# Kernel tuning notes

Hardware: AMD Instinct MI355X
Metric: run time of the kernel (lower is better)

Reference implementation:

```python
import jax, jax.numpy as jnp
import numpy as np

N_NODES = 50000
N_EDGES = 800000
D = 64


def setup_inputs() -> dict:
    key = jax.random.key(0)
    k1, k2, k3 = jax.random.split(key, 3)
    x = jax.random.normal(k1, (N_NODES, D), dtype=jnp.float32)
    edge_index = jax.random.randint(k2, (2, N_EDGES), 0, N_NODES, dtype=jnp.int64)
    # GCNConv linear weight (PyG stores lin.weight [out, in]; we use [in, out])
    W = jax.random.normal(k3, (D, D), dtype=jnp.float32) * (1.0 / np.sqrt(D))
    b = jnp.zeros((D,), dtype=jnp.float32)
    return {"x": x, "edge_index": edge_index, "W": W, "b": b}


def reference(x, edge_index, W, b):
    # ResidualGCNLayer forward (eval mode: dropout = identity).
    # in_channels == out_channels -> skip_connection is Identity.
    N = x.shape[0]
    E = edge_index.shape[1]
    dtype = x.dtype

    # GCNConv with add_self_loops=True, improved=False (fill value 1.0)
    loop = jnp.arange(N, dtype=edge_index.dtype)
    row = jnp.concatenate([edge_index[0], loop])  # source nodes
    col = jnp.concatenate([edge_index[1], loop])  # destination nodes
    ew = jnp.ones((E + N,), dtype=dtype)          # edge weights (self-loop fill=1)

    # symmetric normalization: D^{-1/2} A_hat D^{-1/2}
    deg = jax.ops.segment_sum(ew, col, num_segments=N)
    dinv = jnp.where(deg > 0, jax.lax.rsqrt(deg), jnp.zeros_like(deg))
    norm = dinv[row] * ew * dinv[col]             # [E+N]

    h = x @ W                                     # [N, D] transform before propagate
    msg = norm[:, None] * h[row]                  # [E+N, D] gathered + scaled messages
    agg = jax.ops.segment_sum(msg, col, num_segments=N)  # scatter-add aggregate

    identity = x                                  # Identity skip (in == out)
    out = jax.nn.relu(agg + b) + identity         # ReLU + (eval) dropout + residual
    return out
```

## Files before the change

### kernel.cpp

```cpp
#include <hip/hip_runtime.h>
#include <hip/hip_bf16.h>

#define D 64
#define CAP 64
#define NXCD 8
#define EPT 4

typedef int v4i __attribute__((ext_vector_type(4)));

__device__ __forceinline__ float bf16lo(unsigned u) {
    u <<= 16; return __builtin_bit_cast(float, u);
}
__device__ __forceinline__ float bf16hi(unsigned u) {
    u &= 0xffff0000u; return __builtin_bit_cast(float, u);
}
__device__ __forceinline__ unsigned bf16_rne(float f) {
    unsigned u = __builtin_bit_cast(unsigned, f);
    u += 0x7fffu + ((u >> 16) & 1u);
    return u >> 16;
}
__device__ __forceinline__ unsigned pack_bf16(float a, float b) {
    return bf16_rne(a) | (bf16_rne(b) << 16);
}

__global__ void zero_cnt_kernel(int* __restrict__ cnt, int N) {
    int i = blockIdx.x * blockDim.x + threadIdx.x;
    if (i < N) cnt[i] = 0;
}

__global__ __launch_bounds__(256) void fill_csr_sliced_kernel(
        const int* __restrict__ row, const int* __restrict__ col,
        int* __restrict__ cnt, int* __restrict__ csr, int E, int N) {
    const int slice = blockIdx.x & (NXCD - 1);
    const int chunk = blockIdx.x >> 3;
    const int per = (N + NXCD - 1) / NXCD;
    const int lo = slice * per;
    const int hi = min(N, lo + per);

    const int e0 = (chunk * 256 + (int)threadIdx.x) * EPT;
    if (e0 + EPT <= E) {
        v4i c4 = __builtin_nontemporal_load((const v4i*)(col + e0));
        #pragma unroll
        for (int i = 0; i < EPT; ++i) {
            int c = c4[i];
            if (c >= lo && c < hi) {
                int r = __builtin_nontemporal_load(row + e0 + i);
                int pos = atomicAdd(&cnt[c], 1);
                if (pos < CAP) csr[c * CAP + pos] = r;
            }
        }
    } else {
        for (int i = 0; i < EPT; ++i) {
            int e = e0 + i;
            if (e < E) {
                int c = col[e];
                if (c >= lo && c < hi) {
                    int pos = atomicAdd(&cnt[c], 1);
                    if (pos < CAP) csr[c * CAP + pos] = row[e];
                }
            }
        }
    }
}

__global__ __launch_bounds__(256) void transform_kernel(
        const float* __restrict__ x, const float* __restrict__ W,
        const int* __restrict__ cnt, unsigned* __restrict__ h2b, int N) {
    __shared__ float Ws[D * D];
    __shared__ float xs[32][68];

    for (int i = threadIdx.x; i < D * D; i += 256) Ws[i] = W[i];

    const int l16 = threadIdx.x & 15;
    const int m   = threadIdx.x >> 4;
    const int base = blockIdx.x * 64;
    const float4* x4 = (const float4*)x;

    for (int pass = 0; pass < 2; ++pass) {
        int nb = base + pass * 32;
        __syncthreads();
        for (int i = threadIdx.x; i < 512; i += 256) {
            int r = i >> 4, seg = i & 15;
            int n = nb + r;
            float4 v = make_float4(0.f, 0.f, 0.f, 0.f);
            if (n < N) v = x4[n * 16 + seg];
            *(float4*)&xs[r][seg * 4] = v;
        }
        __syncthreads();

        float4 acc0 = make_float4(0.f, 0.f, 0.f, 0.f);
        float4 acc1 = make_float4(0.f, 0.f, 0.f, 0.f);
        #pragma unroll 4
        for (int k4 = 0; k4 < 16; ++k4) {
            float4 xv0 = *(const float4*)&xs[m][k4 * 4];
            float4 xv1 = *(const float4*)&xs[m + 16][k4 * 4];
            #pragma unroll
            for (int kk = 0; kk < 4; ++kk) {
                float4 w4 = *(const float4*)&Ws[(k4 * 4 + kk) * D + l16 * 4];
                float a0 = kk == 0 ? xv0.x : kk == 1 ? xv0.y : kk == 2 ? xv0.z : xv0.w;
                float a1 = kk == 0 ? xv1.x : kk == 1 ? xv1.y : kk == 2 ? xv1.z : xv1.w;
                acc0.x = fmaf(a0, w4.x, acc0.x); acc0.y = fmaf(a0, w4.y, acc0.y);
                acc0.z = fmaf(a0, w4.z, acc0.z); acc0.w = fmaf(a0, w4.w, acc0.w);
                acc1.x = fmaf(a1, w4.x, acc1.x); acc1.y = fmaf(a1, w4.y, acc1.y);
                acc1.z = fmaf(a1, w4.z, acc1.z); acc1.w = fmaf(a1, w4.w, acc1.w);
            }
        }

        int n0 = nb + m, n1 = nb + m + 16;
        if (n0 < N) {
            float dn = rsqrtf((float)(cnt[n0] + 1));
            uint2 p; p.x = pack_bf16(acc0.x * dn, acc0.y * dn);
            p.y = pack_bf16(acc0.z * dn, acc0.w * dn);
            ((uint2*)h2b)[n0 * 16 + l16] = p;
        }
        if (n1 < N) {
            float dn = rsqrtf((float)(cnt[n1] + 1));
            uint2 p; p.x = pack_bf16(acc1.x * dn, acc1.y * dn);
            p.y = pack_bf16(acc1.z * dn, acc1.w * dn);
            ((uint2*)h2b)[n1 * 16 + l16] = p;
        }
    }
}

__global__ __launch_bounds__(256) void agg_kernel(
        const float* __restrict__ x, const float* __restrict__ b,
        const unsigned* __restrict__ h2b, const int* __restrict__ cnt,
        const int* __restrict__ csr, float* __restrict__ out, int N) {
    const int l16 = threadIdx.x & 15;
    const int gid = threadIdx.x >> 4;
    const int gw  = gid & 3;
    const int c = blockIdx.x * 16 + gid;
    if (c >= N) return;

    const uint2* hb = (const uint2*)h2b;

    const float4 bv = ((const float4*)b)[l16];
    const float4 xv = ((const float4*)x)[c * 16 + l16];

    uint2 v = hb[c * 16 + l16];
    float4 acc;
    acc.x = bf16lo(v.x); acc.y = bf16hi(v.x);
    acc.z = bf16lo(v.y); acc.w = bf16hi(v.y);

    int n = cnt[c]; n = n < CAP ? n : CAP;
    const int* cb = csr + c * CAP;

    for (int j0 = 0; j0 < n; j0 += 16) {
        int idx = (j0 + l16 < n) ? cb[j0 + l16] : 0;
        int m = n - j0; m = m < 16 ? m : 16;
        #pragma unroll 4
        for (int jj = 0; jj < m; ++jj) {
            int r = __shfl(idx, gw * 16 + jj);
            uint2 w = hb[r * 16 + l16];
            acc.x += bf16lo(w.x); acc.y += bf16hi(w.x);
            acc.z += bf16lo(w.y); acc.w += bf16hi(w.y);
        }
    }

    float dc = rsqrtf((float)(cnt[c] + 1));
    float4 o;
    o.x = fmaf(dc, acc.x, bv.x); o.x = o.x > 0.0f ? o.x : 0.0f; o.x += xv.x;
    o.y = fmaf(dc, acc.y, bv.y); o.y = o.y > 0.0f ? o.y : 0.0f; o.y += xv.y;
    o.z = fmaf(dc, acc.z, bv.z); o.z = o.z > 0.0f ? o.z : 0.0f; o.z += xv.z;
    o.w = fmaf(dc, acc.w, bv.w); o.w = o.w > 0.0f ? o.w : 0.0f; o.w += xv.w;
    ((float4*)out)[c * 16 + l16] = o;
}

extern "C" void kernel_launch(void* const* d_in, const int* in_sizes, int n_in,
                              void* d_out, int out_size, void* d_ws, size_t ws_size,
                              hipStream_t stream) {
    const float* x   = (const float*)d_in[0];
    const int*   ei  = (const int*)d_in[1];
    const float* W   = (const float*)d_in[2];
    const float* b   = (const float*)d_in[3];
    float*       out = (float*)d_out;

    const int N = in_sizes[0] / D;
    const int E = in_sizes[1] / 2;
    const int* row = ei;
    const int* col = ei + E;

    int*      cnt = (int*)d_ws;
    unsigned* h2b = (unsigned*)(cnt + N);
    int*      csr = (int*)(h2b + (size_t)N * D / 2);

    zero_cnt_kernel<<<(N + 255) / 256, 256, 0, stream>>>(cnt, N);

    const int fill_chunks = (E + 256 * EPT - 1) / (256 * EPT);
    fill_csr_sliced_kernel<<<fill_chunks * NXCD, 256, 0, stream>>>(row, col, cnt, csr, E, N);

    transform_kernel<<<(N + 63) / 64, 256, 0, stream>>>(x, W, cnt, h2b, N);
    agg_kernel<<<(N + 15) / 16, 256, 0, stream>>>(x, b, h2b, cnt, csr, out, N);
}
```

Baseline: 156.5 us.

## Fuse four graph-conv kernels into one persistent kernel with grid barriers

Replaces the zero, CSR-fill, transform and aggregate launches with a single persistent kernel of 1024 blocks that loops over the work of each phase and separates phases with a software grid barrier built on an atomic counter. The aim is to remove per-launch overhead and the gaps between the four dispatches. The barrier relies on all 1024 blocks being co-resident, which a normal launch does not guarantee, so it could deadlock. Grid-wide barriers and fewer blocks in the fill and aggregate phases may also cost more than the launch gaps they remove.

Result: slower. 563.7 us (+260.3%).

```diff
diff --git a/kernel.cpp b/kernel.cpp
--- a/kernel.cpp
+++ b/kernel.cpp
@@ -5,6 +5,8 @@
 #define CAP 64
 #define NXCD 8
 #define EPT 4
+#define GRID 1024
+#define TPB 256
 
 typedef int v4i __attribute__((ext_vector_type(4)));
 
@@ -23,147 +25,168 @@
     return bf16_rne(a) | (bf16_rne(b) << 16);
 }
 
-__global__ void zero_cnt_kernel(int* __restrict__ cnt, int N) {
-    int i = blockIdx.x * blockDim.x + threadIdx.x;
-    if (i < N) cnt[i] = 0;
-}
-
-__global__ __launch_bounds__(256) void fill_csr_sliced_kernel(
-        const int* __restrict__ row, const int* __restrict__ col,
-        int* __restrict__ cnt, int* __restrict__ csr, int E, int N) {
-    const int slice = blockIdx.x & (NXCD - 1);
-    const int chunk = blockIdx.x >> 3;
-    const int per = (N + NXCD - 1) / NXCD;
-    const int lo = slice * per;
-    const int hi = min(N, lo + per);
-
-    const int e0 = (chunk * 256 + (int)threadIdx.x) * EPT;
-    if (e0 + EPT <= E) {
-        v4i c4 = __builtin_nontemporal_load((const v4i*)(col + e0));
-        #pragma unroll
-        for (int i = 0; i < EPT; ++i) {
-            int c = c4[i];
-            if (c >= lo && c < hi) {
-                int r = __builtin_nontemporal_load(row + e0 + i);
-                int pos = atomicAdd(&cnt[c], 1);
-                if (pos < CAP) csr[c * CAP + pos] = r;
+__device__ __forceinline__ void grid_sync(unsigned* bar, unsigned target) {
+    __syncthreads();
+    if (threadIdx.x == 0) {
+        __threadfence();
+        atomicAdd(bar, 1u);
+        while (__hip_atomic_load(bar, __ATOMIC_ACQUIRE,
+                                 __HIP_MEMORY_SCOPE_AGENT) < target)
+            __builtin_amdgcn_s_sleep(8);
+        __threadfence();
+    }
+    __syncthreads();
+}
+
+__global__ __launch_bounds__(TPB, 4) void fused_kernel(
+        const float* __restrict__ x, const int* __restrict__ row,
+        const int* __restrict__ col, const float* __restrict__ W,
+        const float* __restrict__ b, int* __restrict__ cnt,
+        unsigned* __restrict__ h2b, int* __restrict__ csr,
+        unsigned* __restrict__ bar, float* __restrict__ out,
+        int N, int E) {
+    __shared__ float Ws[D * D];
+    __shared__ float xs[32][68];
+
+    const int tid = threadIdx.x;
+
+    for (int i = blockIdx.x * TPB + tid; i < N; i += GRID * TPB) cnt[i] = 0;
+    grid_sync(bar, GRID * 1u);
+
+    {
+        const int per = (N + NXCD - 1) / NXCD;
+        const int nch = (E + TPB * EPT - 1) / (TPB * EPT);
+        for (int vw = blockIdx.x; vw < nch * NXCD; vw += GRID) {
+            const int slice = vw & (NXCD - 1);
+            const int chunk = vw >> 3;
+            const int lo = slice * per;
+            const int hi = min(N, lo + per);
+            const int e0 = (chunk * TPB + tid) * EPT;
+            if (e0 + EPT <= E) {
+                v4i c4 = __builtin_nontemporal_load((const v4i*)(col + e0));
+                #pragma unroll
+                for (int i = 0; i < EPT; ++i) {
+                    int c = c4[i];
+                    if (c >= lo && c < hi) {
+                        int r = __builtin_nontemporal_load(row + e0 + i);
+                        int pos = atomicAdd(&cnt[c], 1);
+                        if (pos < CAP) csr[c * CAP + pos] = r;
+                    }
+                }
+            } else {
+                for (int i = 0; i < EPT; ++i) {
+                    int e = e0 + i;
+                    if (e < E) {
+                        int c = col[e];
+                        if (c >= lo && c < hi) {
+                            int pos = atomicAdd(&cnt[c], 1);
+                            if (pos < CAP) csr[c * CAP + pos] = row[e];
+                        }
+                    }
+                }
             }
         }
-    } else {
-        for (int i = 0; i < EPT; ++i) {
-            int e = e0 + i;
-            if (e < E) {
-                int c = col[e];
-                if (c >= lo && c < hi) {
-                    int pos = atomicAdd(&cnt[c], 1);
-                    if (pos < CAP) csr[c * CAP + pos] = row[e];
+    }
+    grid_sync(bar, GRID * 2u);
+
+    for (int i = tid; i < D * D; i += TPB) Ws[i] = W[i];
+    {
+        const int l16 = tid & 15;
+        const int m   = tid >> 4;
+        const float4* x4 = (const float4*)x;
+        const int ntiles = (N + 63) / 64;
+        for (int tile = blockIdx.x; tile < ntiles; tile += GRID) {
+            const int base = tile * 64;
+            for (int pass = 0; pass < 2; ++pass) {
+                int nb = base + pass * 32;
+                __syncthreads();
+                for (int i = tid; i < 512; i += TPB) {
+                    int r = i >> 4, seg = i & 15;
+                    int n = nb + r;
+                    float4 v = make_float4(0.f, 0.f, 0.f, 0.f);
+                    if (n < N) v = x4[n * 16 + seg];
+                    *(float4*)&xs[r][seg * 4] = v;
+                }
+                __syncthreads();
+
+                float4 acc0 = make_float4(0.f, 0.f, 0.f, 0.f);
+                float4 acc1 = make_float4(0.f, 0.f, 0.f, 0.f);
+                #pragma unroll 4
+                for (int k4 = 0; k4 < 16; ++k4) {
+                    float4 xv0 = *(const float4*)&xs[m][k4 * 4];
+                    float4 xv1 = *(const float4*)&xs[m + 16][k4 * 4];
+                    #pragma unroll
+                    for (int kk = 0; kk < 4; ++kk) {
+                        float4 w4 = *(const float4*)&Ws[(k4 * 4 + kk) * D + l16 * 4];
+                        float a0 = kk == 0 ? xv0.x : kk == 1 ? xv0.y : kk == 2 ? xv0.z : xv0.w;
+                        float a1 = kk == 0 ? xv1.x : kk == 1 ? xv1.y : kk == 2 ? xv1.z : xv1.w;
+                        acc0.x = fmaf(a0, w4.x, acc0.x); acc0.y = fmaf(a0, w4.y, acc0.y);
+                        acc0.z = fmaf(a0, w4.z, acc0.z); acc0.w = fmaf(a0, w4.w, acc0.w);
+                        acc1.x = fmaf(a1, w4.x, acc1.x); acc1.y = fmaf(a1, w4.y, acc1.y);
+                        acc1.w = fmaf(a1, w4.w, acc1.w); acc1.z = fmaf(a1, w4.z, acc1.z);
+                    }
+                }
+
+                int n0 = nb + m, n1 = nb + m + 16;
+                if (n0 < N) {
+                    float dn = rsqrtf((float)(cnt[n0] + 1));
+                    uint2 p; p.x = pack_bf16(acc0.x * dn, acc0.y * dn);
+                    p.y = pack_bf16(acc0.z * dn, acc0.w * dn);
+                    ((uint2*)h2b)[n0 * 16 + l16] = p;
+                }
+                if (n1 < N) {
+                    float dn = rsqrtf((float)(cnt[n1] + 1));
+                    uint2 p; p.x = pack_bf16(acc1.x * dn, acc1.y * dn);
+                    p.y = pack_bf16(acc1.z * dn, acc1.w * dn);
+                    ((uint2*)h2b)[n1 * 16 + l16] = p;
                 }
             }
         }
     }
-}
-
-__global__ __launch_bounds__(256) void transform_kernel(
-        const float* __restrict__ x, const float* __restrict__ W,
-        const int* __restrict__ cnt, unsigned* __restrict__ h2b, int N) {
-    __shared__ float Ws[D * D];
-    __shared__ float xs[32][68];
-
-    for (int i = threadIdx.x; i < D * D; i += 256) Ws[i] = W[i];
-
-    const int l16 = threadIdx.x & 15;
-    const int m   = threadIdx.x >> 4;
-    const int base = blockIdx.x * 64;
-    const float4* x4 = (const float4*)x;
-
-    for (int pass = 0; pass < 2; ++pass) {
-        int nb = base + pass * 32;
-        __syncthreads();
-        for (int i = threadIdx.x; i < 512; i += 256) {
-            int r = i >> 4, seg = i & 15;
-            int n = nb + r;
-            float4 v = make_float4(0.f, 0.f, 0.f, 0.f);
-            if (n < N) v = x4[n * 16 + seg];
-            *(float4*)&xs[r][seg * 4] = v;
-        }
-        __syncthreads();
-
-        float4 acc0 = make_float4(0.f, 0.f, 0.f, 0.f);
-        float4 acc1 = make_float4(0.f, 0.f, 0.f, 0.f);
-        #pragma unroll 4
-        for (int k4 = 0; k4 < 16; ++k4) {
-            float4 xv0 = *(const float4*)&xs[m][k4 * 4];
-            float4 xv1 = *(const float4*)&xs[m + 16][k4 * 4];
-            #pragma unroll
-            for (int kk = 0; kk < 4; ++kk) {
-                float4 w4 = *(const float4*)&Ws[(k4 * 4 + kk) * D + l16 * 4];
-                float a0 = kk == 0 ? xv0.x : kk == 1 ? xv0.y : kk == 2 ? xv0.z : xv0.w;
-                float a1 = kk == 0 ? xv1.x : kk == 1 ? xv1.y : kk == 2 ? xv1.z : xv1.w;
-                acc0.x = fmaf(a0, w4.x, acc0.x); acc0.y = fmaf(a0, w4.y, acc0.y);
-                acc0.z = fmaf(a0, w4.z, acc0.z); acc0.w = fmaf(a0, w4.w, acc0.w);
-                acc1.x = fmaf(a1, w4.x, acc1.x); acc1.y = fmaf(a1, w4.y, acc1.y);
-                acc1.z = fmaf(a1, w4.z, acc1.z); acc1.w = fmaf(a1, w4.w, acc1.w);
+    grid_sync(bar, GRID * 3u);
+
+    {
+        const int l16 = tid & 15;
+        const int gid = tid >> 4;
+        const int gw  = gid & 3;
+        const uint2* hb = (const uint2*)h2b;
+        const int ntiles = (N + 15) / 16;
+        for (int tile = blockIdx.x; tile < ntiles; tile += GRID) {
+            const int c = tile * 16 + gid;
+            if (c < N) {
+                const float4 bv = ((const float4*)b)[l16];
+                const float4 xv = ((const float4*)x)[c * 16 + l16];
+
+                uint2 v = hb[c * 16 + l16];
+                float4 acc;
+                acc.x = bf16lo(v.x); acc.y = bf16hi(v.x);
+                acc.z = bf16lo(v.y); acc.w = bf16hi(v.y);
+
+                int n = cnt[c]; n = n < CAP ? n : CAP;
+                const int* cb = csr + c * CAP;
+
+                for (int j0 = 0; j0 < n; j0 += 16) {
+                    int idx = (j0 + l16 < n) ? cb[j0 + l16] : 0;
+                    int m = n - j0; m = m < 16 ? m : 16;
+                    #pragma unroll 4
+                    for (int jj = 0; jj < m; ++jj) {
+                        int r = __shfl(idx, gw * 16 + jj);
+                        uint2 w = hb[r * 16 + l16];
+                        acc.x += bf16lo(w.x); acc.y += bf16hi(w.x);
+                        acc.z += bf16lo(w.y); acc.w += bf16hi(w.y);
+                    }
+                }
+
+                float dc = rsqrtf((float)(cnt[c] + 1));
+                float4 o;
+                o.x = fmaf(dc, acc.x, bv.x); o.x = o.x > 0.0f ? o.x : 0.0f; o.x += xv.x;
+                o.y = fmaf(dc, acc.y, bv.y); o.y = o.y > 0.0f ? o.y : 0.0f; o.y += xv.y;
+                o.z = fmaf(dc, acc.z, bv.z); o.z = o.z > 0.0f ? o.z : 0.0f; o.z += xv.z;
+                o.w = fmaf(dc, acc.w, bv.w); o.w = o.w > 0.0f ? o.w : 0.0f; o.w += xv.w;
+                ((float4*)out)[c * 16 + l16] = o;
             }
         }
-
-        int n0 = nb + m, n1 = nb + m + 16;
-        if (n0 < N) {
-            float dn = rsqrtf((float)(cnt[n0] + 1));
-            uint2 p; p.x = pack_bf16(acc0.x * dn, acc0.y * dn);
-            p.y = pack_bf16(acc0.z * dn, acc0.w * dn);
-            ((uint2*)h2b)[n0 * 16 + l16] = p;
-        }
-        if (n1 < N) {
-            float dn = rsqrtf((float)(cnt[n1] + 1));
-            uint2 p; p.x = pack_bf16(acc1.x * dn, acc1.y * dn);
-            p.y = pack_bf16(acc1.z * dn, acc1.w * dn);
-            ((uint2*)h2b)[n1 * 16 + l16] = p;
-        }
-    }
-}
-
-__global__ __launch_bounds__(256) void agg_kernel(
-        const float* __restrict__ x, const float* __restrict__ b,
-        const unsigned* __restrict__ h2b, const int* __restrict__ cnt,
-        const int* __restrict__ csr, float* __restrict__ out, int N) {
-    const int l16 = threadIdx.x & 15;
-    const int gid = threadIdx.x >> 4;
-    const int gw  = gid & 3;
-    const int c = blockIdx.x * 16 + gid;
-    if (c >= N) return;
-
-    const uint2* hb = (const uint2*)h2b;
-
-    const float4 bv = ((const float4*)b)[l16];
-    const float4 xv = ((const float4*)x)[c * 16 + l16];
-
-    uint2 v = hb[c * 16 + l16];
-    float4 acc;
-    acc.x = bf16lo(v.x); acc.y = bf16hi(v.x);
-    acc.z = bf16lo(v.y); acc.w = bf16hi(v.y);
-
-    int n = cnt[c]; n = n < CAP ? n : CAP;
-    const int* cb = csr + c * CAP;
-
-    for (int j0 = 0; j0 < n; j0 += 16) {
-        int idx = (j0 + l16 < n) ? cb[j0 + l16] : 0;
-        int m = n - j0; m = m < 16 ? m : 16;
-        #pragma unroll 4
-        for (int jj = 0; jj < m; ++jj) {
-            int r = __shfl(idx, gw * 16 + jj);
-            uint2 w = hb[r * 16 + l16];
-            acc.x += bf16lo(w.x); acc.y += bf16hi(w.x);
-            acc.z += bf16lo(w.y); acc.w += bf16hi(w.y);
-        }
-    }
-
-    float dc = rsqrtf((float)(cnt[c] + 1));
-    float4 o;
-    o.x = fmaf(dc, acc.x, bv.x); o.x = o.x > 0.0f ? o.x : 0.0f; o.x += xv.x;
-    o.y = fmaf(dc, acc.y, bv.y); o.y = o.y > 0.0f ? o.y : 0.0f; o.y += xv.y;
-    o.z = fmaf(dc, acc.z, bv.z); o.z = o.z > 0.0f ? o.z : 0.0f; o.z += xv.z;
-    o.w = fmaf(dc, acc.w, bv.w); o.w = o.w > 0.0f ? o.w : 0.0f; o.w += xv.w;
-    ((float4*)out)[c * 16 + l16] = o;
+    }
 }
 
 extern "C" void kernel_launch(void* const* d_in, const int* in_sizes, int n_in,
@@ -183,12 +206,9 @@
     int*      cnt = (int*)d_ws;
     unsigned* h2b = (unsigned*)(cnt + N);
     int*      csr = (int*)(h2b + (size_t)N * D / 2);
-
-    zero_cnt_kernel<<<(N + 255) / 256, 256, 0, stream>>>(cnt, N);
-
-    const int fill_chunks = (E + 256 * EPT - 1) / (256 * EPT);
-    fill_csr_sliced_kernel<<<fill_chunks * NXCD, 256, 0, stream>>>(row, col, cnt, csr, E, N);
-
-    transform_kernel<<<(N + 63) / 64, 256, 0, stream>>>(x, W, cnt, h2b, N);
-    agg_kernel<<<(N + 15) / 16, 256, 0, stream>>>(x, b, h2b, cnt, csr, out, N);
-}
+    unsigned* bar = (unsigned*)(csr + (size_t)N * CAP);
+
+    hipMemsetAsync(bar, 0, sizeof(unsigned), stream);
+    fused_kernel<<<GRID, TPB, 0, stream>>>(x, row, col, W, b, cnt, h2b, csr,
+                                           bar, out, N, E);
+}
```
